# Optimization experiments

Measured on AMD Instinct MI355X. Metric: run time of the kernel, lower is better.

## Reference

```python
import jax, jax.numpy as jnp
import numpy as np

N_GROUP = 8
TOPK_GROUP = 4
TOP_K = 8
ROUTED_SCALING = 2.5
NUM_EXPERTS = 256
HIDDEN = 7168
TOKENS = 8192


def setup_inputs() -> dict:
    key = jax.random.key(0)
    k1, k2, k3 = jax.random.split(key, 3)
    hidden_states = jax.random.normal(k1, (TOKENS, HIDDEN), dtype=jnp.float32)
    weight = jax.random.normal(k2, (NUM_EXPERTS, HIDDEN), dtype=jnp.float32) * 0.02
    e_score_correction_bias = jax.random.normal(k3, (NUM_EXPERTS,), dtype=jnp.float32) * 0.1
    return {"hidden_states": hidden_states, "weight": weight,
            "e_score_correction_bias": e_score_correction_bias}


def reference(hidden_states, weight, e_score_correction_bias):
    # logits = x @ W^T  (fp32 gate GEMM)
    logits = jnp.einsum('th,eh->te', hidden_states.astype(jnp.float32), weight)
    scores = jax.nn.sigmoid(logits)                       # [T, E]
    swb = scores + e_score_correction_bias                # [T, E]
    T, E = swb.shape
    gsize = E // N_GROUP
    # per-group score = sum of top-2 biased scores within each group
    grouped = swb.reshape(T, N_GROUP, gsize)
    top2, _ = jax.lax.top_k(grouped, 2)                   # [T, G, 2]
    group_scores = top2.sum(axis=-1)                      # [T, G]
    # keep topk_group groups
    _, gidx = jax.lax.top_k(group_scores, TOPK_GROUP)     # [T, topk_group]
    rows = jnp.arange(T)[:, None]
    group_mask = jnp.zeros((T, N_GROUP), jnp.float32).at[rows, gidx].set(1.0)
    score_mask = jnp.repeat(group_mask, gsize, axis=-1)   # [T, E]
    swb_masked = swb * score_mask
    # top_k experts among kept groups
    _, tidx = jax.lax.top_k(swb_masked, TOP_K)            # [T, top_k]
    new_mask = jnp.zeros((T, E), jnp.float32).at[rows, tidx].set(1.0)
    sel = scores * new_mask
    score_sum = sel.sum(axis=-1, keepdims=True) + 1e-20
    return sel / score_sum * ROUTED_SCALING
```

## Files before the change

### kernel.cpp

```cpp
#include <hip/hip_runtime.h>
#include <math.h>

#define TOKENS   8192
#define HIDDEN   7168
#define NEXPERT  256
#define NGROUP   8
#define TOPKG    4
#define TOPK     8
#define SCALE    2.5f

#define BM 128
#define BN 128
#define BK 32
#define KSPLIT 4
#define KPB (HIDDEN / KSPLIT)
#define NT  (KPB / BK)

#define RSTR 72

typedef _Float16 half8 __attribute__((ext_vector_type(8)));
typedef _Float16 half4 __attribute__((ext_vector_type(4)));
typedef float    floatx4 __attribute__((ext_vector_type(4)));

__device__ __forceinline__ void cvt_store(_Float16* __restrict__ H,
                                          int row, int k0, float4 v) {
    half4 h, l;
    h[0] = (_Float16)v.x; h[1] = (_Float16)v.y;
    h[2] = (_Float16)v.z; h[3] = (_Float16)v.w;
    l[0] = (_Float16)(v.x - (float)h[0]);
    l[1] = (_Float16)(v.y - (float)h[1]);
    l[2] = (_Float16)(v.z - (float)h[2]);
    l[3] = (_Float16)(v.w - (float)h[3]);
    const int base = row * RSTR + ((k0 >> 3) << 4) + (k0 & 7);
    *(half4*)&H[base]     = h;
    *(half4*)&H[base + 8] = l;
}

__global__ __launch_bounds__(256) void zero_kernel(float* __restrict__ O) {
    const int i = blockIdx.x * 256 + threadIdx.x;
    *(float4*)&O[(size_t)i * 4] = float4{0.f, 0.f, 0.f, 0.f};
}

__global__ __launch_bounds__(256, 2) void gate_gemm_kernel(
    const float* __restrict__ X, const float* __restrict__ W,
    float* __restrict__ OUT)
{
    __shared__ _Float16 Ab[2][BM * RSTR];
    __shared__ _Float16 Bb[2][BN * RSTR];

    const int tid = threadIdx.x;
    const int nb  = blockIdx.x * BN;
    const int mb  = blockIdx.y * BM;
    const int kb  = blockIdx.z * KPB;

    const int srow = tid >> 3;
    const int sk0  = (tid & 7) * 4;
    const float* Aptr = X + (size_t)(mb + srow) * HIDDEN + kb + sk0;
    const float* Bptr = W + (size_t)(nb + srow) * HIDDEN + kb + sk0;

    float4 av[4], bv[4];
#pragma unroll
    for (int q = 0; q < 4; q++) {
        av[q] = *(const float4*)(Aptr + (size_t)(q * 32) * HIDDEN);
        bv[q] = *(const float4*)(Bptr + (size_t)(q * 32) * HIDDEN);
    }
#pragma unroll
    for (int q = 0; q < 4; q++) {
        cvt_store(Ab[0], q * 32 + srow, sk0, av[q]);
        cvt_store(Bb[0], q * 32 + srow, sk0, bv[q]);
    }

    const int lane = tid & 63, wave = tid >> 6;
    const int wm = (wave >> 1) * 64, wn = (wave & 1) * 64;
    const int fr = lane & 15, quad = lane >> 4;

    floatx4 acc[4][4];
#pragma unroll
    for (int i = 0; i < 4; i++)
#pragma unroll
        for (int j = 0; j < 4; j++) acc[i][j] = floatx4{0.f, 0.f, 0.f, 0.f};

    for (int t = 0; t < NT; t++) {
        if (t + 1 < NT) {
            const int o = (t + 1) * BK;
#pragma unroll
            for (int q = 0; q < 4; q++) {
                av[q] = *(const float4*)(Aptr + o + (size_t)(q * 32) * HIDDEN);
                bv[q] = *(const float4*)(Bptr + o + (size_t)(q * 32) * HIDDEN);
            }
        }

        __syncthreads();

        const _Float16* __restrict__ Ac = Ab[t & 1];
        const _Float16* __restrict__ Bc = Bb[t & 1];

        half8 ah[4], al[4];
#pragma unroll
        for (int i = 0; i < 4; i++) {
            const int a = (wm + i * 16 + fr) * RSTR + quad * 16;
            ah[i] = *(const half8*)&Ac[a];
            al[i] = *(const half8*)&Ac[a + 8];
        }
#pragma unroll
        for (int j = 0; j < 4; j++) {
            const int b = (wn + j * 16 + fr) * RSTR + quad * 16;
            const half8 bh = *(const half8*)&Bc[b];
            const half8 bl = *(const half8*)&Bc[b + 8];
#pragma unroll
            for (int i = 0; i < 4; i++) {
                acc[i][j] = __builtin_amdgcn_mfma_f32_16x16x32_f16(
                    al[i], bh, acc[i][j], 0, 0, 0);
                acc[i][j] = __builtin_amdgcn_mfma_f32_16x16x32_f16(
                    ah[i], bl, acc[i][j], 0, 0, 0);
                acc[i][j] = __builtin_amdgcn_mfma_f32_16x16x32_f16(
                    ah[i], bh, acc[i][j], 0, 0, 0);
            }
        }

        if (t + 1 < NT) {
            _Float16* An = Ab[(t + 1) & 1];
            _Float16* Bn = Bb[(t + 1) & 1];
#pragma unroll
            for (int q = 0; q < 4; q++) {
                cvt_store(An, q * 32 + srow, sk0, av[q]);
                cvt_store(Bn, q * 32 + srow, sk0, bv[q]);
            }
        }
    }

#pragma unroll
    for (int i = 0; i < 4; i++)
#pragma unroll
        for (int j = 0; j < 4; j++) {
            const int col = nb + wn + j * 16 + fr;
#pragma unroll
            for (int r = 0; r < 4; r++) {
                const int row = mb + wm + i * 16 + quad * 4 + r;
                atomicAdd(&OUT[(size_t)row * NEXPERT + col], acc[i][j][r]);
            }
        }
}

__global__ __launch_bounds__(256) void route_kernel(
    float* __restrict__ S, const float* __restrict__ bias)
{
    const int lane = threadIdx.x & 63;
    const int wave = threadIdx.x >> 6;
    const int t    = blockIdx.x * 4 + wave;

    const float4 lg4 = *(const float4*)&S[(size_t)t * NEXPERT + lane * 4];
    const float4 b4  = *(const float4*)&bias[lane * 4];
    float sc[4];
    sc[0] = 1.0f / (1.0f + expf(-lg4.x));
    sc[1] = 1.0f / (1.0f + expf(-lg4.y));
    sc[2] = 1.0f / (1.0f + expf(-lg4.z));
    sc[3] = 1.0f / (1.0f + expf(-lg4.w));
    float swb[4] = { sc[0] + b4.x, sc[1] + b4.y, sc[2] + b4.z, sc[3] + b4.w };

    float m1 = -INFINITY, m2 = -INFINITY;
#pragma unroll
    for (int j = 0; j < 4; j++) {
        const float v = swb[j];
        if (v > m1)      { m2 = m1; m1 = v; }
        else if (v > m2) { m2 = v; }
    }
#pragma unroll
    for (int s = 1; s < 8; s <<= 1) {
        const float o1 = __shfl_xor(m1, s, 64);
        const float o2 = __shfl_xor(m2, s, 64);
        const float hi = fmaxf(m1, o1);
        const float lo = fminf(m1, o1);
        m2 = fmaxf(lo, fmaxf(m2, o2));
        m1 = hi;
    }
    const float gs = m1 + m2;

    float gsc[NGROUP];
#pragma unroll
    for (int g = 0; g < NGROUP; g++) gsc[g] = __shfl(gs, g * 8, 64);
    const int myg = lane >> 3;
    int rank = 0;
#pragma unroll
    for (int g = 0; g < NGROUP; g++)
        rank += (gsc[g] > gs) || (gsc[g] == gs && g < myg);
    const bool kept = (rank < TOPKG);

    float v[4];
#pragma unroll
    for (int j = 0; j < 4; j++) v[j] = kept ? swb[j] : 0.0f;

    float sum = 0.0f;
    int selmask = 0;
    for (int r = 0; r < TOPK; r++) {
        float bv = -INFINITY;
        int   bi = 0x7fffffff;
#pragma unroll
        for (int j = 0; j < 4; j++) {
            const bool avail = ((selmask >> j) & 1) == 0;
            if (avail && v[j] > bv) { bv = v[j]; bi = lane * 4 + j; }
        }
#pragma unroll
        for (int s = 1; s < 64; s <<= 1) {
            const float ov = __shfl_xor(bv, s, 64);
            const int   oi = __shfl_xor(bi, s, 64);
            if (ov > bv || (ov == bv && oi < bi)) { bv = ov; bi = oi; }
        }
        const int wl = bi >> 2, wj = bi & 3;
        const float mysc = (wj == 0) ? sc[0] : (wj == 1) ? sc[1]
                         : (wj == 2) ? sc[2] : sc[3];
        sum += __shfl(mysc, wl, 64);
        if (lane == wl) selmask |= (1 << wj);
    }

    const float rcp = SCALE / (sum + 1e-20f);
    float4 o;
    o.x = (selmask & 1) ? sc[0] * rcp : 0.0f;
    o.y = (selmask & 2) ? sc[1] * rcp : 0.0f;
    o.z = (selmask & 4) ? sc[2] * rcp : 0.0f;
    o.w = (selmask & 8) ? sc[3] * rcp : 0.0f;
    *(float4*)&S[(size_t)t * NEXPERT + lane * 4] = o;
}

extern "C" void kernel_launch(void* const* d_in, const int* in_sizes, int n_in,
                              void* d_out, int out_size, void* d_ws, size_t ws_size,
                              hipStream_t stream) {
    const float* X    = (const float*)d_in[0];
    const float* W    = (const float*)d_in[1];
    const float* bias = (const float*)d_in[2];
    float* out = (float*)d_out;
    (void)d_ws; (void)ws_size;

    zero_kernel<<<(TOKENS * NEXPERT / 4) / 256, 256, 0, stream>>>(out);
    dim3 ggrid(NEXPERT / BN, TOKENS / BM, KSPLIT);
    gate_gemm_kernel<<<ggrid, 256, 0, stream>>>(X, W, out);
    route_kernel<<<TOKENS / 4, 256, 0, stream>>>(out, bias);
}
```

Before: 385.8 us.

## Pre-split weights into swizzled fp16 tiles and DMA them directly to LDS

Adds a pre-pass kernel that converts the gate weight into hi/lo fp16 pairs, laid out as pre-tiled, XOR-swizzled 16KB LDS images in workspace. The GEMM then streams B tiles with global_load_lds DMA instead of loading fp32, converting and storing them per block. The A path moves to 8-element chunks in the same swizzled layout, replacing the padded row stride. This removes the repeated weight conversion done by every token tile and cuts register and VALU pressure, at the cost of an extra kernel launch and workspace traffic. It also relies on the hardware ordering the asynchronous LDS DMA correctly with respect to the single barrier per iteration.

```diff
diff --git a/kernel.cpp b/kernel.cpp
--- a/kernel.cpp
+++ b/kernel.cpp
@@ -15,25 +15,28 @@
 #define KSPLIT 4
 #define KPB (HIDDEN / KSPLIT)
 #define NT  (KPB / BK)
-
-#define RSTR 72
+#define TILE_BYTES 16384
+
 
 typedef _Float16 half8 __attribute__((ext_vector_type(8)));
-typedef _Float16 half4 __attribute__((ext_vector_type(4)));
 typedef float    floatx4 __attribute__((ext_vector_type(4)));
 
-__device__ __forceinline__ void cvt_store(_Float16* __restrict__ H,
-                                          int row, int k0, float4 v) {
-    half4 h, l;
-    h[0] = (_Float16)v.x; h[1] = (_Float16)v.y;
-    h[2] = (_Float16)v.z; h[3] = (_Float16)v.w;
-    l[0] = (_Float16)(v.x - (float)h[0]);
-    l[1] = (_Float16)(v.y - (float)h[1]);
-    l[2] = (_Float16)(v.z - (float)h[2]);
-    l[3] = (_Float16)(v.w - (float)h[3]);
-    const int base = row * RSTR + ((k0 >> 3) << 4) + (k0 & 7);
-    *(half4*)&H[base]     = h;
-    *(half4*)&H[base + 8] = l;
+__device__ __forceinline__ void cvt8(const float4 a, const float4 b,
+                                     half8& h, half8& l) {
+    h[0] = (_Float16)a.x; h[1] = (_Float16)a.y;
+    h[2] = (_Float16)a.z; h[3] = (_Float16)a.w;
+    h[4] = (_Float16)b.x; h[5] = (_Float16)b.y;
+    h[6] = (_Float16)b.z; h[7] = (_Float16)b.w;
+    l[0] = (_Float16)(a.x - (float)h[0]); l[1] = (_Float16)(a.y - (float)h[1]);
+    l[2] = (_Float16)(a.z - (float)h[2]); l[3] = (_Float16)(a.w - (float)h[3]);
+    l[4] = (_Float16)(b.x - (float)h[4]); l[5] = (_Float16)(b.y - (float)h[5]);
+    l[6] = (_Float16)(b.z - (float)h[6]); l[7] = (_Float16)(b.w - (float)h[7]);
+}
+
+__device__ __forceinline__ void lds_dma16(const char* g, char* l) {
+    __builtin_amdgcn_global_load_lds(
+        (const __attribute__((address_space(1))) void*)g,
+        (__attribute__((address_space(3))) void*)l, 16, 0, 0);
 }
 
 __global__ __launch_bounds__(256) void zero_kernel(float* __restrict__ O) {
@@ -41,39 +44,69 @@
     *(float4*)&O[(size_t)i * 4] = float4{0.f, 0.f, 0.f, 0.f};
 }
 
+__global__ __launch_bounds__(896) void wsplit_kernel(
+    const float* __restrict__ W, char* __restrict__ WS)
+{
+    const int e  = blockIdx.x;
+    const int og = threadIdx.x;
+    const float4 a = *(const float4*)&W[(size_t)e * HIDDEN + og * 8];
+    const float4 b = *(const float4*)&W[(size_t)e * HIDDEN + og * 8 + 4];
+    half8 h, l;
+    cvt8(a, b, h, l);
+
+    const int kz  = og / 224;
+    const int tt  = (og % 224) >> 2;
+    const int oc  = og & 3;
+    const int row = e & 127, nb = e >> 7;
+    char* base = WS + (size_t)((nb * KSPLIT + kz) * NT + tt) * TILE_BYTES;
+    const int b0 = (row * 128 + oc * 32) ^ ((row & 7) << 4);
+    *(half8*)(base + b0)        = h;
+    *(half8*)(base + (b0 ^ 16)) = l;
+}
+
 __global__ __launch_bounds__(256, 2) void gate_gemm_kernel(
-    const float* __restrict__ X, const float* __restrict__ W,
+    const float* __restrict__ X, const char* __restrict__ WS,
     float* __restrict__ OUT)
 {
-    __shared__ _Float16 Ab[2][BM * RSTR];
-    __shared__ _Float16 Bb[2][BN * RSTR];
+    __shared__ __attribute__((aligned(128))) char Ab[2][TILE_BYTES];
+    __shared__ __attribute__((aligned(128))) char Bb[2][TILE_BYTES];
 
     const int tid = threadIdx.x;
     const int nb  = blockIdx.x * BN;
     const int mb  = blockIdx.y * BM;
     const int kb  = blockIdx.z * KPB;
 
-    const int srow = tid >> 3;
-    const int sk0  = (tid & 7) * 4;
-    const float* Aptr = X + (size_t)(mb + srow) * HIDDEN + kb + sk0;
-    const float* Bptr = W + (size_t)(nb + srow) * HIDDEN + kb + sk0;
-
-    float4 av[4], bv[4];
-#pragma unroll
-    for (int q = 0; q < 4; q++) {
-        av[q] = *(const float4*)(Aptr + (size_t)(q * 32) * HIDDEN);
-        bv[q] = *(const float4*)(Bptr + (size_t)(q * 32) * HIDDEN);
-    }
-#pragma unroll
-    for (int q = 0; q < 4; q++) {
-        cvt_store(Ab[0], q * 32 + srow, sk0, av[q]);
-        cvt_store(Bb[0], q * 32 + srow, sk0, bv[q]);
-    }
+    const int arow = tid >> 2;
+    const int aoct = tid & 3;
+    const float* Aptr = X + (size_t)(mb + arow) * HIDDEN + kb + aoct * 8;
+    const int ab0 = (arow * 128 + aoct * 32) ^ ((arow & 7) << 4);
+
+    const char* Wimg =
+        WS + (size_t)((blockIdx.x * KSPLIT + blockIdx.z) * NT) * TILE_BYTES;
 
     const int lane = tid & 63, wave = tid >> 6;
     const int wm = (wave >> 1) * 64, wn = (wave & 1) * 64;
     const int fr = lane & 15, quad = lane >> 4;
 
+    {
+        const char* src = Wimg + wave * 4096 + lane * 16;
+        char* dst = &Bb[0][wave * 4096];
+#pragma unroll
+        for (int c = 0; c < 4; c++)
+            lds_dma16(src + c * 1024, dst + c * 1024);
+
+#pragma unroll
+        for (int p = 0; p < 2; p++) {
+            const float4 a = *(const float4*)(Aptr + (size_t)p * 64 * HIDDEN);
+            const float4 b = *(const float4*)(Aptr + (size_t)p * 64 * HIDDEN + 4);
+            half8 h, l;
+            cvt8(a, b, h, l);
+            const int off = ab0 + p * 8192;
+            *(half8*)&Ab[0][off]      = h;
+            *(half8*)&Ab[0][off ^ 16] = l;
+        }
+    }
+
     floatx4 acc[4][4];
 #pragma unroll
     for (int i = 0; i < 4; i++)
@@ -81,32 +114,41 @@
         for (int j = 0; j < 4; j++) acc[i][j] = floatx4{0.f, 0.f, 0.f, 0.f};
 
     for (int t = 0; t < NT; t++) {
+        __syncthreads();
+
+        const int cur = t & 1, nxt = (t + 1) & 1;
+        float4 na0, nb0, na1, nb1;
         if (t + 1 < NT) {
-            const int o = (t + 1) * BK;
-#pragma unroll
-            for (int q = 0; q < 4; q++) {
-                av[q] = *(const float4*)(Aptr + o + (size_t)(q * 32) * HIDDEN);
-                bv[q] = *(const float4*)(Bptr + o + (size_t)(q * 32) * HIDDEN);
-            }
-        }
-
-        __syncthreads();
-
-        const _Float16* __restrict__ Ac = Ab[t & 1];
-        const _Float16* __restrict__ Bc = Bb[t & 1];
+            const float* ap = Aptr + (t + 1) * BK;
+            na0 = *(const float4*)(ap);
+            nb0 = *(const float4*)(ap + 4);
+            na1 = *(const float4*)(ap + (size_t)64 * HIDDEN);
+            nb1 = *(const float4*)(ap + (size_t)64 * HIDDEN + 4);
+            const char* src = Wimg + (size_t)(t + 1) * TILE_BYTES
+                            + wave * 4096 + lane * 16;
+            char* dst = &Bb[nxt][wave * 4096];
+#pragma unroll
+            for (int c = 0; c < 4; c++)
+                lds_dma16(src + c * 1024, dst + c * 1024);
+        }
+
+        const char* Ac = Ab[cur];
+        const char* Bc = Bb[cur];
 
         half8 ah[4], al[4];
 #pragma unroll
         for (int i = 0; i < 4; i++) {
-            const int a = (wm + i * 16 + fr) * RSTR + quad * 16;
-            ah[i] = *(const half8*)&Ac[a];
-            al[i] = *(const half8*)&Ac[a + 8];
+            const int r = wm + i * 16 + fr;
+            const int o = (r * 128 + quad * 32) ^ ((r & 7) << 4);
+            ah[i] = *(const half8*)&Ac[o];
+            al[i] = *(const half8*)&Ac[o ^ 16];
         }
 #pragma unroll
         for (int j = 0; j < 4; j++) {
-            const int b = (wn + j * 16 + fr) * RSTR + quad * 16;
-            const half8 bh = *(const half8*)&Bc[b];
-            const half8 bl = *(const half8*)&Bc[b + 8];
+            const int r = wn + j * 16 + fr;
+            const int o = (r * 128 + quad * 32) ^ ((r & 7) << 4);
+            const half8 bh = *(const half8*)&Bc[o];
+            const half8 bl = *(const half8*)&Bc[o ^ 16];
 #pragma unroll
             for (int i = 0; i < 4; i++) {
                 acc[i][j] = __builtin_amdgcn_mfma_f32_16x16x32_f16(
@@ -119,13 +161,13 @@
         }
 
         if (t + 1 < NT) {
-            _Float16* An = Ab[(t + 1) & 1];
-            _Float16* Bn = Bb[(t + 1) & 1];
-#pragma unroll
-            for (int q = 0; q < 4; q++) {
-                cvt_store(An, q * 32 + srow, sk0, av[q]);
-                cvt_store(Bn, q * 32 + srow, sk0, bv[q]);
-            }
+            half8 h, l;
+            cvt8(na0, nb0, h, l);
+            *(half8*)&Ab[nxt][ab0]      = h;
+            *(half8*)&Ab[nxt][ab0 ^ 16] = l;
+            cvt8(na1, nb1, h, l);
+            *(half8*)&Ab[nxt][(ab0 + 8192)]      = h;
+            *(half8*)&Ab[nxt][(ab0 + 8192) ^ 16] = l;
         }
     }
 
@@ -229,10 +271,11 @@
     const float* W    = (const float*)d_in[1];
     const float* bias = (const float*)d_in[2];
     float* out = (float*)d_out;
-    (void)d_ws; (void)ws_size;
+    char* ws = (char*)d_ws; (void)ws_size;
 
     zero_kernel<<<(TOKENS * NEXPERT / 4) / 256, 256, 0, stream>>>(out);
+    wsplit_kernel<<<NEXPERT, 896, 0, stream>>>(W, ws);
     dim3 ggrid(NEXPERT / BN, TOKENS / BM, KSPLIT);
-    gate_gemm_kernel<<<ggrid, 256, 0, stream>>>(X, W, out);
+    gate_gemm_kernel<<<ggrid, 256, 0, stream>>>(X, ws, out);
     route_kernel<<<TOKENS / 4, 256, 0, stream>>>(out, bias);
 }
```

After: 408.1 us. 1.06x slower.

## Pre-split weight into fp16 hi/lo tile images in a separate kernel

Applied to the files above, without the earlier changes.

Adds a kernel that converts the gate weight once per call into fp16 high/low pairs, stored in a tile-contiguous workspace layout matching the GEMM's shared-memory staging. The GEMM then loads B tiles as ready-made half8 pairs instead of reloading fp32 weights and converting them in every block. This removes redundant conversion work and halves nothing in bytes (hi+lo fp16 equals fp32 size) but makes the loads contiguous. It costs an extra kernel launch and a workspace write/read of the weight.

```diff
diff --git a/kernel.cpp b/kernel.cpp
--- a/kernel.cpp
+++ b/kernel.cpp
@@ -15,6 +15,7 @@
 #define KSPLIT 4
 #define KPB (HIDDEN / KSPLIT)
 #define NT  (KPB / BK)
+#define TILE_BYTES 16384
 
 #define RSTR 72
 
@@ -36,13 +37,45 @@
     *(half4*)&H[base + 8] = l;
 }
 
+__device__ __forceinline__ void cvt8(const float4 a, const float4 b,
+                                     half8& h, half8& l) {
+    h[0] = (_Float16)a.x; h[1] = (_Float16)a.y;
+    h[2] = (_Float16)a.z; h[3] = (_Float16)a.w;
+    h[4] = (_Float16)b.x; h[5] = (_Float16)b.y;
+    h[6] = (_Float16)b.z; h[7] = (_Float16)b.w;
+    l[0] = (_Float16)(a.x - (float)h[0]); l[1] = (_Float16)(a.y - (float)h[1]);
+    l[2] = (_Float16)(a.z - (float)h[2]); l[3] = (_Float16)(a.w - (float)h[3]);
+    l[4] = (_Float16)(b.x - (float)h[4]); l[5] = (_Float16)(b.y - (float)h[5]);
+    l[6] = (_Float16)(b.z - (float)h[6]); l[7] = (_Float16)(b.w - (float)h[7]);
+}
+
 __global__ __launch_bounds__(256) void zero_kernel(float* __restrict__ O) {
     const int i = blockIdx.x * 256 + threadIdx.x;
     *(float4*)&O[(size_t)i * 4] = float4{0.f, 0.f, 0.f, 0.f};
 }
 
+__global__ __launch_bounds__(896) void wsplit_kernel(
+    const float* __restrict__ W, char* __restrict__ WS)
+{
+    const int e  = blockIdx.x;
+    const int og = threadIdx.x;
+    const float4 a = *(const float4*)&W[(size_t)e * HIDDEN + og * 8];
+    const float4 b = *(const float4*)&W[(size_t)e * HIDDEN + og * 8 + 4];
+    half8 h, l;
+    cvt8(a, b, h, l);
+
+    const int kz  = og / 224;
+    const int tt  = (og % 224) >> 2;
+    const int oc  = og & 3;
+    const int row = e & 127, nb = e >> 7;
+    char* p = WS + (size_t)((nb * KSPLIT + kz) * NT + tt) * TILE_BYTES
+            + (row * 4 + oc) * 32;
+    *(half8*)p        = h;
+    *(half8*)(p + 16) = l;
+}
+
 __global__ __launch_bounds__(256, 2) void gate_gemm_kernel(
-    const float* __restrict__ X, const float* __restrict__ W,
+    const float* __restrict__ X, const char* __restrict__ WS,
     float* __restrict__ OUT)
 {
     __shared__ _Float16 Ab[2][BM * RSTR];
@@ -56,18 +89,32 @@
     const int srow = tid >> 3;
     const int sk0  = (tid & 7) * 4;
     const float* Aptr = X + (size_t)(mb + srow) * HIDDEN + kb + sk0;
-    const float* Bptr = W + (size_t)(nb + srow) * HIDDEN + kb + sk0;
-
-    float4 av[4], bv[4];
-#pragma unroll
-    for (int q = 0; q < 4; q++) {
+
+    const char* Wimg =
+        WS + (size_t)((blockIdx.x * KSPLIT + blockIdx.z) * NT) * TILE_BYTES;
+    const int brow[2] = { tid >> 2, (tid + 256) >> 2 };
+    const int boct    = tid & 3;
+    const int bbase[2] = { brow[0] * RSTR + boct * 16,
+                           brow[1] * RSTR + boct * 16 };
+
+    float4 av[4];
+    half8  nh[2], nl[2];
+#pragma unroll
+    for (int q = 0; q < 4; q++)
         av[q] = *(const float4*)(Aptr + (size_t)(q * 32) * HIDDEN);
-        bv[q] = *(const float4*)(Bptr + (size_t)(q * 32) * HIDDEN);
-    }
-#pragma unroll
-    for (int q = 0; q < 4; q++) {
+#pragma unroll
+    for (int s = 0; s < 2; s++) {
+        const char* src = Wimg + (tid + 256 * s) * 32;
+        nh[s] = *(const half8*)src;
+        nl[s] = *(const half8*)(src + 16);
+    }
+#pragma unroll
+    for (int q = 0; q < 4; q++)
         cvt_store(Ab[0], q * 32 + srow, sk0, av[q]);
-        cvt_store(Bb[0], q * 32 + srow, sk0, bv[q]);
+#pragma unroll
+    for (int s = 0; s < 2; s++) {
+        *(half8*)&Bb[0][bbase[s]]     = nh[s];
+        *(half8*)&Bb[0][bbase[s] + 8] = nl[s];
     }
 
     const int lane = tid & 63, wave = tid >> 6;
@@ -84,9 +131,14 @@
         if (t + 1 < NT) {
             const int o = (t + 1) * BK;
 #pragma unroll
-            for (int q = 0; q < 4; q++) {
+            for (int q = 0; q < 4; q++)
                 av[q] = *(const float4*)(Aptr + o + (size_t)(q * 32) * HIDDEN);
-                bv[q] = *(const float4*)(Bptr + o + (size_t)(q * 32) * HIDDEN);
+            const char* srcT = Wimg + (size_t)(t + 1) * TILE_BYTES;
+#pragma unroll
+            for (int s = 0; s < 2; s++) {
+                const char* src = srcT + (tid + 256 * s) * 32;
+                nh[s] = *(const half8*)src;
+                nl[s] = *(const half8*)(src + 16);
             }
         }
 
@@ -122,9 +174,12 @@
             _Float16* An = Ab[(t + 1) & 1];
             _Float16* Bn = Bb[(t + 1) & 1];
 #pragma unroll
-            for (int q = 0; q < 4; q++) {
+            for (int q = 0; q < 4; q++)
                 cvt_store(An, q * 32 + srow, sk0, av[q]);
-                cvt_store(Bn, q * 32 + srow, sk0, bv[q]);
+#pragma unroll
+            for (int s = 0; s < 2; s++) {
+                *(half8*)&Bn[bbase[s]]     = nh[s];
+                *(half8*)&Bn[bbase[s] + 8] = nl[s];
             }
         }
     }
@@ -229,10 +284,11 @@
     const float* W    = (const float*)d_in[1];
     const float* bias = (const float*)d_in[2];
     float* out = (float*)d_out;
-    (void)d_ws; (void)ws_size;
+    char* ws = (char*)d_ws; (void)ws_size;
 
     zero_kernel<<<(TOKENS * NEXPERT / 4) / 256, 256, 0, stream>>>(out);
+    wsplit_kernel<<<NEXPERT, 896, 0, stream>>>(W, ws);
     dim3 ggrid(NEXPERT / BN, TOKENS / BM, KSPLIT);
-    gate_gemm_kernel<<<ggrid, 256, 0, stream>>>(X, W, out);
+    gate_gemm_kernel<<<ggrid, 256, 0, stream>>>(X, ws, out);
     route_kernel<<<TOKENS / 4, 256, 0, stream>>>(out, bias);
 }
```

Result: no change. 385.2 us (-0.2%).
